# Kernel tuning notes

Hardware: AMD Instinct MI355X
Metric: run time of the kernel (lower is better)

The kernel has to match this reference:

```python
import jax, jax.numpy as jnp
import numpy as np


def setup_inputs() -> dict:
    key = jax.random.key(0)
    k1, k2, k3 = jax.random.split(key, 3)
    N, C_in, H, W = 32, 16, 256, 256
    C_out, K = 64, 3
    x = jax.random.normal(k1, (N, C_in, H, W), dtype=jnp.float32)
    # match nn.Conv2d default init scale roughly (values irrelevant for correctness harness)
    fan_in = C_in * K * K
    bound = 1.0 / np.sqrt(fan_in)
    conv_weight = jax.random.normal(k2, (C_out, C_in, K, K), dtype=jnp.float32) * bound
    conv_bias = jax.random.normal(k3, (C_out,), dtype=jnp.float32) * bound
    return {"x": x, "conv_weight": conv_weight, "conv_bias": conv_bias}


def reference(x, conv_weight, conv_bias):
    # Conv2d: stride=1, padding=0 (VALID), dilation=1, groups=1
    y = jax.lax.conv_general_dilated(
        x, conv_weight,
        window_strides=(1, 1), padding='VALID',
        dimension_numbers=('NCHW', 'OIHW', 'NCHW'),
    ) + conv_bias[None, :, None, None]          # (N, C_out, OH, OW)
    y = jnp.min(y, axis=1, keepdims=True)       # min over output channels -> (N, 1, OH, OW)
    return jnp.tanh(jnp.tanh(y))                # double tanh
```

## Files before the change

### kernel.cpp

```cpp
#include <hip/hip_runtime.h>
#include <hip/hip_bf16.h>

typedef __attribute__((ext_vector_type(8)))  short short8;
typedef __attribute__((ext_vector_type(4)))  float f32x4;
typedef __attribute__((ext_vector_type(16))) float f32x16;

#define CIN   16
#define HH    256
#define WW    256
#define OHH   254
#define OWW   254
#define HW    (HH * WW)

#define SLOTU  (36 * 8)
#define HALF_R (16 * SLOTU + 8)

__device__ __forceinline__ ushort f2bf(float f) {
    unsigned u = __builtin_bit_cast(unsigned, f);
    unsigned r = (u + 0x7fffu + ((u >> 16) & 1u)) >> 16;
    return (ushort)r;
}

__device__ __forceinline__ float dtanh2(float x) {
    const float K = 2.8853900817779268f;
    float xc = fminf(fmaxf(x, -9.0f), 9.0f);
    float e1 = __builtin_amdgcn_exp2f(K * xc);
    float t1 = 1.0f - 2.0f * __builtin_amdgcn_rcpf(e1 + 1.0f);
    float e2 = __builtin_amdgcn_exp2f(K * t1);
    return 1.0f - 2.0f * __builtin_amdgcn_rcpf(e2 + 1.0f);
}

__device__ __forceinline__ float rmin16(f32x16 a) {
    float t0 = fminf(fminf(a[0],  a[1]),  fminf(a[2],  a[3]));
    float t1 = fminf(fminf(a[4],  a[5]),  fminf(a[6],  a[7]));
    float t2 = fminf(fminf(a[8],  a[9]),  fminf(a[10], a[11]));
    float t3 = fminf(fminf(a[12], a[13]), fminf(a[14], a[15]));
    return fminf(fminf(t0, t1), fminf(t2, t3));
}

__global__ void prep_weights(const float* __restrict__ wsrc, ushort* __restrict__ wfrag) {
    int idx = blockIdx.x * 256 + threadIdx.x;
    if (idx >= 9216) return;
    int r    = idx & 7;
    int lane = (idx >> 3) & 63;
    int j    = (idx >> 9) & 1;
    int tap  = idx >> 10;
    int ci   = 8 * (lane >> 5) + r;
    int co   = j * 32 + (lane & 31);
    int kh   = tap / 3, kw = tap - 3 * kh;
    wfrag[idx] = f2bf(wsrc[(co * CIN + ci) * 9 + kh * 3 + kw]);
}

__global__ __launch_bounds__(256, 4) void conv_min_tanh(
        const float* __restrict__ x, const ushort* __restrict__ wfrag,
        const float* __restrict__ bias, float* __restrict__ out) {
    __shared__ ushort ring[2 * HALF_R];
    __shared__ ushort mp[2][2][4][32];

    const int tid   = threadIdx.x;
    const int ow0   = blockIdx.x * 32;
    const int hbase = blockIdx.y * 64;
    const int n     = blockIdx.z;
    const float* xb = x + (size_t)n * CIN * HW;

    auto stage_inline = [&](int pos) {
        int lr_  = pos / 36;
        int rm_  = pos - lr_ * 36;
        int ciq_ = rm_ / 9;
        int w4_  = rm_ - ciq_ * 9;
        int hg  = min(hbase + lr_, HH - 1);
        int wg_ = min(ow0 + 4 * w4_, WW - 4);
        const float* src = xb + (size_t)(ciq_ * 4) * HW + hg * WW + wg_;
        f32x4 v0 = *reinterpret_cast<const f32x4*>(src);
        f32x4 v1 = *reinterpret_cast<const f32x4*>(src + HW);
        f32x4 v2 = *reinterpret_cast<const f32x4*>(src + 2 * HW);
        f32x4 v3 = *reinterpret_cast<const f32x4*>(src + 3 * HW);
        ushort* dst = &ring[(ciq_ >> 1) * HALF_R + lr_ * SLOTU + (4 * w4_) * 8 + (ciq_ & 1) * 4];
#pragma unroll
        for (int e = 0; e < 4; ++e) {
            unsigned lo, hi;
            asm("v_cvt_pk_bf16_f32 %0, %1, %2" : "=v"(lo) : "v"(v0[e]), "v"(v1[e]));
            asm("v_cvt_pk_bf16_f32 %0, %1, %2" : "=v"(hi) : "v"(v2[e]), "v"(v3[e]));
            uint2 pk; pk.x = lo; pk.y = hi;
            *reinterpret_cast<uint2*>(dst + e * 8) = pk;
        }
    };
    stage_inline(tid);
    if (tid < 32) stage_inline(tid + 256);

    const bool sa = (tid < 144);
    const int lr  = tid / 36;
    const int rm  = tid - lr * 36;
    const int ciq = rm / 9;
    const int w4  = rm - ciq * 9;
    const int wg  = min(ow0 + 4 * w4, WW - 4);
    const float* gbase = xb + (size_t)(ciq * 4) * HW + wg;
    ushort* sdst = &ring[(ciq >> 1) * HALF_R + (4 * w4) * 8 + (ciq & 1) * 4];

    f32x4 ra0 = {}, ra1 = {}, ra2 = {}, ra3 = {};

#define ISSUE(cc)                                                              \
    if (sa) {                                                                  \
        int hg = min(hbase + 4 * (cc) + lr, HH - 1);                           \
        const float* s_ = gbase + hg * WW;                                     \
        asm volatile("global_load_dwordx4 %0, %1, off" : "=v"(ra0) : "v"(s_) : "memory");           \
        asm volatile("global_load_dwordx4 %0, %1, off" : "=v"(ra1) : "v"(s_ + HW) : "memory");      \
        asm volatile("global_load_dwordx4 %0, %1, off" : "=v"(ra2) : "v"(s_ + 2 * HW) : "memory");  \
        asm volatile("global_load_dwordx4 %0, %1, off" : "=v"(ra3) : "v"(s_ + 3 * HW) : "memory");  \
    }

#define WRITEBK(cc)                                                            \
    if (sa) {                                                                  \
        ushort* d_ = sdst + ((4 * (cc) + lr) & 15) * SLOTU;                    \
        _Pragma("unroll")                                                      \
        for (int e = 0; e < 4; ++e) {                                          \
            unsigned lo_, hi_;                                                 \
            asm("v_cvt_pk_bf16_f32 %0, %1, %2" : "=v"(lo_) : "v"(ra0[e]), "v"(ra1[e]));  \
            asm("v_cvt_pk_bf16_f32 %0, %1, %2" : "=v"(hi_) : "v"(ra2[e]), "v"(ra3[e]));  \
            uint2 pk_; pk_.x = lo_; pk_.y = hi_;                               \
            *reinterpret_cast<uint2*>(d_ + e * 8) = pk_;                       \
        }                                                                      \
    }

    ISSUE(2);

    const int lane  = tid & 63;
    const int wid   = tid >> 6;
    const int jw    = wid & 1;
    const int rq    = wid >> 1;
    const int px    = lane & 31;
    const int khalf = lane >> 5;
    short8 wf[9];
#pragma unroll
    for (int tap = 0; tap < 9; ++tap)
        wf[tap] = *reinterpret_cast<const short8*>(wfrag + ((tap * 2 + jw) * 64 + lane) * 8);
    f32x16 bi;
#pragma unroll
    for (int q4 = 0; q4 < 4; ++q4) {
        f32x4 b = *reinterpret_cast<const f32x4*>(bias + jw * 32 + 4 * khalf + 8 * q4);
#pragma unroll
        for (int s = 0; s < 4; ++s) bi[q4 * 4 + s] = b[s];
    }
    const ushort* bptr = &ring[khalf * HALF_R + px * 8];

    asm volatile("s_waitcnt lgkmcnt(0)" ::: "memory");
    __builtin_amdgcn_s_barrier();

#pragma unroll 2
    for (int c = 0; c < 16; ++c) {
        {
            const int R0 = 4 * c + 2 * rq;
            f32x16 a0 = bi, a1 = bi;
#pragma unroll
            for (int t = 0; t < 4; ++t) {
                const ushort* rp = bptr + ((R0 + t) & 15) * SLOTU;
                short8 f0 = *reinterpret_cast<const short8*>(rp);
                short8 f1 = *reinterpret_cast<const short8*>(rp + 8);
                short8 f2 = *reinterpret_cast<const short8*>(rp + 16);
                if (t < 3) {
                    a0 = __builtin_amdgcn_mfma_f32_32x32x16_bf16(wf[t * 3 + 0], f0, a0, 0, 0, 0);
                    a0 = __builtin_amdgcn_mfma_f32_32x32x16_bf16(wf[t * 3 + 1], f1, a0, 0, 0, 0);
                    a0 = __builtin_amdgcn_mfma_f32_32x32x16_bf16(wf[t * 3 + 2], f2, a0, 0, 0, 0);
                }
                if (t >= 1) {
                    a1 = __builtin_amdgcn_mfma_f32_32x32x16_bf16(wf[(t - 1) * 3 + 0], f0, a1, 0, 0, 0);
                    a1 = __builtin_amdgcn_mfma_f32_32x32x16_bf16(wf[(t - 1) * 3 + 1], f1, a1, 0, 0, 0);
                    a1 = __builtin_amdgcn_mfma_f32_32x32x16_bf16(wf[(t - 1) * 3 + 2], f2, a1, 0, 0, 0);
                }
            }
            float v0 = rmin16(a0), v1 = rmin16(a1);
            v0 = fminf(v0, __shfl_xor(v0, 32, 64));
            v1 = fminf(v1, __shfl_xor(v1, 32, 64));
            if (lane < 32) {
                mp[c & 1][jw][2 * rq + 0][px] = f2bf(v0);
                mp[c & 1][jw][2 * rq + 1][px] = f2bf(v1);
            }
        }

        if (c < 15) {
            asm volatile("s_waitcnt vmcnt(0)"
                         : "+v"(ra0), "+v"(ra1), "+v"(ra2), "+v"(ra3) :: "memory");
            WRITEBK(c + 2);
            ISSUE(min(c + 3, 16));
        }

        asm volatile("s_waitcnt lgkmcnt(0)" ::: "memory");
        __builtin_amdgcn_s_barrier();

        if (tid < 128) {
            const int r4 = tid >> 5, opx = tid & 31;
            float f0 = __builtin_bit_cast(float, (unsigned)mp[c & 1][0][r4][opx] << 16);
            float f1 = __builtin_bit_cast(float, (unsigned)mp[c & 1][1][r4][opx] << 16);
            float y  = dtanh2(fminf(f0, f1));
            const int oh = hbase + 4 * c + r4;
            const int ow = ow0 + opx;
            if (oh < OHH && ow < OWW)
                out[((size_t)n * OHH + oh) * OWW + ow] = y;
        }
    }
#undef ISSUE
#undef WRITEBK
}

extern "C" void kernel_launch(void* const* d_in, const int* in_sizes, int n_in,
                              void* d_out, int out_size, void* d_ws, size_t ws_size,
                              hipStream_t stream) {
    const float* x = (const float*)d_in[0];
    const float* w = (const float*)d_in[1];
    const float* b = (const float*)d_in[2];
    float* out     = (float*)d_out;
    ushort* wfrag  = (ushort*)d_ws;

    prep_weights<<<36, 256, 0, stream>>>(w, wfrag);
    dim3 grid(8, 4, 32);
    conv_min_tanh<<<grid, dim3(256, 1, 1), 0, stream>>>(x, wfrag, b, out);
}
```

Measured before the change: 53.47 us.

## Double rows per block and per iteration with deeper 32-row LDS ring

```diff
diff --git a/kernel.cpp b/kernel.cpp
--- a/kernel.cpp
+++ b/kernel.cpp
@@ -13,7 +13,7 @@
 #define HW    (HH * WW)
 
 #define SLOTU  (36 * 8)
-#define HALF_R (16 * SLOTU + 8)
+#define HALF_R (32 * SLOTU + 8)
 
 __device__ __forceinline__ ushort f2bf(float f) {
     unsigned u = __builtin_bit_cast(unsigned, f);
@@ -51,15 +51,15 @@
     wfrag[idx] = f2bf(wsrc[(co * CIN + ci) * 9 + kh * 3 + kw]);
 }
 
-__global__ __launch_bounds__(256, 4) void conv_min_tanh(
+__global__ __launch_bounds__(256, 2) void conv_min_tanh(
         const float* __restrict__ x, const ushort* __restrict__ wfrag,
         const float* __restrict__ bias, float* __restrict__ out) {
     __shared__ ushort ring[2 * HALF_R];
-    __shared__ ushort mp[2][2][4][32];
+    __shared__ ushort mp[2][2][8][32];
 
     const int tid   = threadIdx.x;
     const int ow0   = blockIdx.x * 32;
-    const int hbase = blockIdx.y * 64;
+    const int hbase = blockIdx.y * 128;
     const int n     = blockIdx.z;
     const float* xb = x + (size_t)n * CIN * HW;
 
@@ -75,7 +75,7 @@
         f32x4 v1 = *reinterpret_cast<const f32x4*>(src + HW);
         f32x4 v2 = *reinterpret_cast<const f32x4*>(src + 2 * HW);
         f32x4 v3 = *reinterpret_cast<const f32x4*>(src + 3 * HW);
-        ushort* dst = &ring[(ciq_ >> 1) * HALF_R + lr_ * SLOTU + (4 * w4_) * 8 + (ciq_ & 1) * 4];
+        ushort* dst = &ring[(ciq_ >> 1) * HALF_R + (lr_ & 31) * SLOTU + (4 * w4_) * 8 + (ciq_ & 1) * 4];
 #pragma unroll
         for (int e = 0; e < 4; ++e) {
             unsigned lo, hi;
@@ -86,32 +86,45 @@
         }
     };
     stage_inline(tid);
-    if (tid < 32) stage_inline(tid + 256);
-
-    const bool sa = (tid < 144);
-    const int lr  = tid / 36;
-    const int rm  = tid - lr * 36;
-    const int ciq = rm / 9;
-    const int w4  = rm - ciq * 9;
-    const int wg  = min(ow0 + 4 * w4, WW - 4);
-    const float* gbase = xb + (size_t)(ciq * 4) * HW + wg;
-    ushort* sdst = &ring[(ciq >> 1) * HALF_R + (4 * w4) * 8 + (ciq & 1) * 4];
+    if (tid < 104) stage_inline(tid + 256);
+
+    const int lra  = tid / 36;
+    const int rma  = tid - lra * 36;
+    const int ciqa = rma / 9;
+    const int w4a  = rma - ciqa * 9;
+    const float* gba = xb + (size_t)(ciqa * 4) * HW + min(ow0 + 4 * w4a, WW - 4);
+    ushort* sda = &ring[(ciqa >> 1) * HALF_R + (4 * w4a) * 8 + (ciqa & 1) * 4];
+    const bool hasb = (tid < 32);
+    const int rmb  = 4 + tid;
+    const int ciqb = rmb / 9;
+    const int w4b  = rmb - ciqb * 9;
+    const float* gbb = xb + (size_t)(ciqb * 4) * HW + min(ow0 + 4 * w4b, WW - 4);
+    ushort* sdb = &ring[(ciqb >> 1) * HALF_R + (4 * w4b) * 8 + (ciqb & 1) * 4];
 
     f32x4 ra0 = {}, ra1 = {}, ra2 = {}, ra3 = {};
+    f32x4 rb0 = {}, rb1 = {}, rb2 = {}, rb3 = {};
 
 #define ISSUE(cc)                                                              \
-    if (sa) {                                                                  \
-        int hg = min(hbase + 4 * (cc) + lr, HH - 1);                           \
-        const float* s_ = gbase + hg * WW;                                     \
+    {                                                                          \
+        int hg = min(hbase + 8 * (cc) + 2 + lra, HH - 1);                      \
+        const float* s_ = gba + hg * WW;                                       \
         asm volatile("global_load_dwordx4 %0, %1, off" : "=v"(ra0) : "v"(s_) : "memory");           \
         asm volatile("global_load_dwordx4 %0, %1, off" : "=v"(ra1) : "v"(s_ + HW) : "memory");      \
         asm volatile("global_load_dwordx4 %0, %1, off" : "=v"(ra2) : "v"(s_ + 2 * HW) : "memory");  \
         asm volatile("global_load_dwordx4 %0, %1, off" : "=v"(ra3) : "v"(s_ + 3 * HW) : "memory");  \
+        if (hasb) {                                                            \
+            int hg2 = min(hbase + 8 * (cc) + 2 + 7, HH - 1);                   \
+            const float* t_ = gbb + hg2 * WW;                                  \
+            asm volatile("global_load_dwordx4 %0, %1, off" : "=v"(rb0) : "v"(t_) : "memory");           \
+            asm volatile("global_load_dwordx4 %0, %1, off" : "=v"(rb1) : "v"(t_ + HW) : "memory");      \
+            asm volatile("global_load_dwordx4 %0, %1, off" : "=v"(rb2) : "v"(t_ + 2 * HW) : "memory");  \
+            asm volatile("global_load_dwordx4 %0, %1, off" : "=v"(rb3) : "v"(t_ + 3 * HW) : "memory");  \
+        }                                                                      \
     }
 
 #define WRITEBK(cc)                                                            \
-    if (sa) {                                                                  \
-        ushort* d_ = sdst + ((4 * (cc) + lr) & 15) * SLOTU;                    \
+    {                                                                          \
+        ushort* d_ = sda + ((8 * (cc) + 2 + lra) & 31) * SLOTU;                \
         _Pragma("unroll")                                                      \
         for (int e = 0; e < 4; ++e) {                                          \
             unsigned lo_, hi_;                                                 \
@@ -120,9 +133,20 @@
             uint2 pk_; pk_.x = lo_; pk_.y = hi_;                               \
             *reinterpret_cast<uint2*>(d_ + e * 8) = pk_;                       \
         }                                                                      \
-    }
-
-    ISSUE(2);
+        if (hasb) {                                                            \
+            ushort* d2 = sdb + ((8 * (cc) + 9) & 31) * SLOTU;                  \
+            _Pragma("unroll")                                                  \
+            for (int e = 0; e < 4; ++e) {                                      \
+                unsigned lo_, hi_;                                             \
+                asm("v_cvt_pk_bf16_f32 %0, %1, %2" : "=v"(lo_) : "v"(rb0[e]), "v"(rb1[e]));  \
+                asm("v_cvt_pk_bf16_f32 %0, %1, %2" : "=v"(hi_) : "v"(rb2[e]), "v"(rb3[e]));  \
+                uint2 pk_; pk_.x = lo_; pk_.y = hi_;                           \
+                *reinterpret_cast<uint2*>(d2 + e * 8) = pk_;                   \
+            }                                                                  \
+        }                                                                      \
+    }
+
+    ISSUE(1);
 
     const int lane  = tid & 63;
     const int wid   = tid >> 6;
@@ -149,50 +173,53 @@
 #pragma unroll 2
     for (int c = 0; c < 16; ++c) {
         {
-            const int R0 = 4 * c + 2 * rq;
-            f32x16 a0 = bi, a1 = bi;
-#pragma unroll
-            for (int t = 0; t < 4; ++t) {
-                const ushort* rp = bptr + ((R0 + t) & 15) * SLOTU;
+            const int P0 = 8 * c + rq * 4;
+            f32x16 a0 = bi, a1 = bi, a2 = bi, a3 = bi;
+#pragma unroll
+            for (int t = 0; t < 6; ++t) {
+                const ushort* rp = bptr + ((P0 + t) & 31) * SLOTU;
                 short8 f0 = *reinterpret_cast<const short8*>(rp);
                 short8 f1 = *reinterpret_cast<const short8*>(rp + 8);
                 short8 f2 = *reinterpret_cast<const short8*>(rp + 16);
-                if (t < 3) {
-                    a0 = __builtin_amdgcn_mfma_f32_32x32x16_bf16(wf[t * 3 + 0], f0, a0, 0, 0, 0);
-                    a0 = __builtin_amdgcn_mfma_f32_32x32x16_bf16(wf[t * 3 + 1], f1, a0, 0, 0, 0);
-                    a0 = __builtin_amdgcn_mfma_f32_32x32x16_bf16(wf[t * 3 + 2], f2, a0, 0, 0, 0);
+#define FEED(i)                                                                         \
+                if (t - (i) >= 0 && t - (i) <= 2) {                                     \
+                    a##i = __builtin_amdgcn_mfma_f32_32x32x16_bf16(wf[(t - (i)) * 3 + 0], f0, a##i, 0, 0, 0); \
+                    a##i = __builtin_amdgcn_mfma_f32_32x32x16_bf16(wf[(t - (i)) * 3 + 1], f1, a##i, 0, 0, 0); \
+                    a##i = __builtin_amdgcn_mfma_f32_32x32x16_bf16(wf[(t - (i)) * 3 + 2], f2, a##i, 0, 0, 0); \
                 }
-                if (t >= 1) {
-                    a1 = __builtin_amdgcn_mfma_f32_32x32x16_bf16(wf[(t - 1) * 3 + 0], f0, a1, 0, 0, 0);
-                    a1 = __builtin_amdgcn_mfma_f32_32x32x16_bf16(wf[(t - 1) * 3 + 1], f1, a1, 0, 0, 0);
-                    a1 = __builtin_amdgcn_mfma_f32_32x32x16_bf16(wf[(t - 1) * 3 + 2], f2, a1, 0, 0, 0);
-                }
+                FEED(0) FEED(1) FEED(2) FEED(3)
+#undef FEED
             }
-            float v0 = rmin16(a0), v1 = rmin16(a1);
+            float v0 = rmin16(a0), v1 = rmin16(a1), v2 = rmin16(a2), v3 = rmin16(a3);
             v0 = fminf(v0, __shfl_xor(v0, 32, 64));
             v1 = fminf(v1, __shfl_xor(v1, 32, 64));
+            v2 = fminf(v2, __shfl_xor(v2, 32, 64));
+            v3 = fminf(v3, __shfl_xor(v3, 32, 64));
             if (lane < 32) {
-                mp[c & 1][jw][2 * rq + 0][px] = f2bf(v0);
-                mp[c & 1][jw][2 * rq + 1][px] = f2bf(v1);
+                mp[c & 1][jw][rq * 4 + 0][px] = f2bf(v0);
+                mp[c & 1][jw][rq * 4 + 1][px] = f2bf(v1);
+                mp[c & 1][jw][rq * 4 + 2][px] = f2bf(v2);
+                mp[c & 1][jw][rq * 4 + 3][px] = f2bf(v3);
             }
         }
 
         if (c < 15) {
             asm volatile("s_waitcnt vmcnt(0)"
-                         : "+v"(ra0), "+v"(ra1), "+v"(ra2), "+v"(ra3) :: "memory");
-            WRITEBK(c + 2);
-            ISSUE(min(c + 3, 16));
+                         : "+v"(ra0), "+v"(ra1), "+v"(ra2), "+v"(ra3),
+                           "+v"(rb0), "+v"(rb1), "+v"(rb2), "+v"(rb3) :: "memory");
+            WRITEBK(c + 1);
+            if (c + 2 <= 15) ISSUE(c + 2);
         }
 
         asm volatile("s_waitcnt lgkmcnt(0)" ::: "memory");
         __builtin_amdgcn_s_barrier();
 
-        if (tid < 128) {
-            const int r4 = tid >> 5, opx = tid & 31;
-            float f0 = __builtin_bit_cast(float, (unsigned)mp[c & 1][0][r4][opx] << 16);
-            float f1 = __builtin_bit_cast(float, (unsigned)mp[c & 1][1][r4][opx] << 16);
+        {
+            const int r8 = tid >> 5, opx = tid & 31;
+            float f0 = __builtin_bit_cast(float, (unsigned)mp[c & 1][0][r8][opx] << 16);
+            float f1 = __builtin_bit_cast(float, (unsigned)mp[c & 1][1][r8][opx] << 16);
             float y  = dtanh2(fminf(f0, f1));
-            const int oh = hbase + 4 * c + r4;
+            const int oh = hbase + 8 * c + r8;
             const int ow = ow0 + opx;
             if (oh < OHH && ow < OWW)
                 out[((size_t)n * OHH + oh) * OWW + ow] = y;
@@ -212,6 +239,6 @@
     ushort* wfrag  = (ushort*)d_ws;
 
     prep_weights<<<36, 256, 0, stream>>>(w, wfrag);
-    dim3 grid(8, 4, 32);
+    dim3 grid(8, 2, 32);
     conv_min_tanh<<<grid, dim3(256, 1, 1), 0, stream>>>(x, wfrag, b, out);
 }
```

After: 52.07 us. 2.6% less time.
